# Performance work log

Measured on AMD Instinct MI355X. Metric: run time of the kernel, lower is better.

The kernel has to match this reference:

```python
import jax, jax.numpy as jnp
import numpy as np

B, R, N, D = 8, 5, 1024, 512  # batch, relations, utterances per dialogue, d_model
LN_EPS = 1e-5


def setup_inputs() -> dict:
    key = jax.random.key(0)
    k1, k2, k3 = jax.random.split(key, 3)
    h = jax.random.normal(k1, (B, N, D), dtype=jnp.float32)
    # Binary adjacency: adj[b, r, v, u] = 1 means u sends a message to v under relation r.
    adj = (jax.random.uniform(k2, (B, R, N, N)) < 0.5).astype(jnp.float32)
    # Relation 0 is the self-loop relation (identity), as in build_adjacency.
    adj = adj.at[:, 0].set(jnp.broadcast_to(jnp.eye(N, dtype=jnp.float32), (B, N, N)))
    # Per-relation Linear (bias=False) weights, torch convention: y = x @ W_r.T, W_r: (D, D)
    W = jax.random.normal(k3, (R, D, D), dtype=jnp.float32) * 0.02
    gamma = jnp.ones((D,), dtype=jnp.float32)
    beta = jnp.zeros((D,), dtype=jnp.float32)
    return {"h": h, "adj": adj, "W": W, "gamma": gamma, "beta": beta}


def reference(h, adj, W, gamma, beta):
    # Degree-normalize each relation's adjacency (row-normalized mean aggregation).
    deg = jnp.clip(jnp.sum(adj, axis=-1, keepdims=True), 1.0)  # (B,R,N,1)
    A = adj / deg
    # Mean aggregation per relation: (B,R,N,N) @ (B,N,D) -> (B,R,N,D)
    msg = jnp.einsum('brvu,bud->brvd', A, h)
    # Per-relation linear (x @ W_r.T) and sum over relations: (B,N,D)
    agg = jnp.einsum('brvd,red->bve', msg, W)
    # Dropout is identity in eval mode; ReLU, residual, LayerNorm.
    out = jax.nn.relu(agg) + h
    mu = jnp.mean(out, axis=-1, keepdims=True)
    xc = out - mu
    var = jnp.mean(xc * xc, axis=-1, keepdims=True)
    return xc / jnp.sqrt(var + LN_EPS) * gamma + beta
```

## Files before the change

### kernel.cpp

```cpp
#include <hip/hip_runtime.h>
#include <stdint.h>

#define Bd 8
#define Rr 5
#define Nn 1024
#define Dd 512
#define KK (Rr*Dd)

typedef __attribute__((ext_vector_type(8))) short bf16x8;
typedef __attribute__((ext_vector_type(4))) float f32x4;
typedef unsigned short u16;
typedef unsigned int u32;

__device__ __forceinline__ u16 f2bf(float x){
  union { float f; unsigned u; } v; v.f = x;
  unsigned r = v.u + 0x7FFFu + ((v.u >> 16) & 1u);
  return (u16)(r >> 16);
}

__global__ __launch_bounds__(256) void k_prep(
    const float* __restrict__ h, const float* __restrict__ W,
    u16* __restrict__ hTp, u16* __restrict__ Wt2p){
  __shared__ float t32[32][65];
  const int tid = threadIdx.x;
  const int g = blockIdx.x;
  if (g < 2048){
    const int ut  = g & 31;
    const int dtg = (g >> 5) & 7;
    const int b   = g >> 8;
    const float* hb = h + ((size_t)b*Nn + (size_t)ut*32)*Dd + dtg*64;
    #pragma unroll
    for (int j=0;j<8;j++){
      int e = j*256 + tid;
      int ul = e >> 6, dl = e & 63;
      t32[ul][dl] = hb[(size_t)ul*Dd + dl];
    }
    __syncthreads();
    u16* ob = hTp + (size_t)b*Dd*Nn;
    #pragma unroll
    for (int j=0;j<8;j++){
      int e = j*256 + tid;
      int dtl = e >> 9;
      int rem = e & 511;
      int dr = rem >> 5, uu = rem & 31;
      int dt = dtg*4 + dtl;
      ob[((size_t)ut*32 + dt)*512 + rem] = f2bf(t32[uu][dtl*16 + dr]);
    }
  } else {
    int q = (g - 2048)*1024 + tid*4;
    int kk = q & 31;
    int er = (q >> 5) & 15;
    int et = (q >> 9) & 31;
    int kt = q >> 14;
    int k = kt*32 + kk;
    int e = et*16 + er;
    int r, d;
    if (k < 2048){ r = 1 + (k >> 9); d = k & 511; }
    else         { r = 0;            d = k - 2048; }
    f32x4 w = *(const f32x4*)(W + (((size_t)r*Dd + e)*Dd + d));
    u16 o[4] = { f2bf(w.x), f2bf(w.y), f2bf(w.z), f2bf(w.w) };
    *(uint2*)(Wt2p + q) = *(uint2*)o;
  }
}

__global__ __launch_bounds__(512,2) void k_fused(
    const float* __restrict__ adj, const u16* __restrict__ hTp,
    const u16* __restrict__ Wt2p, const float* __restrict__ h,
    const float* __restrict__ gamma, const float* __restrict__ beta,
    float* __restrict__ out){
  __shared__ __align__(16) u16 sA[2][4][32*64];
  __shared__ __align__(16) u16 sBt[32*512];
  __shared__ float sT[16*516];
  __shared__ float sDeg[4][32];

  const int tid  = threadIdx.x;
  const int lane = tid & 63;
  const int wave = tid >> 6;
  const int b  = blockIdx.x & 7;
  const int vt = blockIdx.x >> 3;
  const int v0 = vt * 32;
  const int t0 = blockIdx.x & 15;
  const float* adjb = adj + (((size_t)b*Rr + 1)*Nn + v0)*Nn;
  const u16* hTpb = hTp + (size_t)b*Dd*Nn;

  const int srow = tid >> 4;
  const int sc   = tid & 15;
  const size_t aoff = (size_t)srow*Nn + sc*4;
  const int wslot = sc ^ ((srow & 7) << 1);

  float deg[4] = {0.f,0.f,0.f,0.f};
  f32x4 areg[4];
  f32x4 acc[4][2][4];
  #pragma unroll
  for (int ri=0;ri<4;ri++)
    #pragma unroll
    for (int m=0;m<2;m++)
      #pragma unroll
      for (int n=0;n<4;n++) acc[ri][m][n] = (f32x4){0.f,0.f,0.f,0.f};

  const int rlo = lane & 15, ch = lane >> 4;
  const int boff = rlo*32 + ch*8;

  #define TT(x) (((x) + t0) & 15)

  #define AISSUE(T) do {                                                      \
    _Pragma("unroll")                                                         \
    for (int ri=0;ri<4;ri++)                                                  \
      areg[ri] = *(const f32x4*)(adjb + (size_t)ri*Nn*Nn + (size_t)(T)*64 + aoff); \
  } while(0)

  #define PACK(BUFI) do {                                                     \
    _Pragma("unroll")                                                         \
    for (int ri=0;ri<4;ri++){                                                 \
      f32x4 p = areg[ri];                                                     \
      deg[ri] += p.x+p.y+p.z+p.w;                                             \
      uint2 pk;                           \
      pk.x = (__float_as_uint(p.x)>>16) | (__float_as_uint(p.y) & 0xFFFF0000u);\
      pk.y = (__float_as_uint(p.z)>>16) | (__float_as_uint(p.w) & 0xFFFF0000u);\
      *(uint2*)((char*)sA[BUFI][ri] + srow*128 + wslot*8) = pk;               \
    }                                                                         \
  } while(0)

  #define LOADB(T) do {                                                      \
    _Pragma("unroll")                                                         \
    for (int kk=0;kk<2;kk++){                                                 \
      const u16* bp = hTpb + ((((size_t)((T)*2+kk))*32 + (wave<<2))<<9) + boff;\
      _Pragma("unroll")                                                       \
      for (int n=0;n<4;n++)                                                   \
        bfr[kk][n] = *(const bf16x8*)(bp + ((size_t)n<<9));                   \
    }                                                                         \
  } while(0)

  #define MSTEP(BUFI) do {                                                    \
    const char* abase = (const char*)sA[BUFI];                                \
    _Pragma("unroll")                                                         \
    for (int kk=0;kk<2;kk++){                                                 \
      _Pragma("unroll")                                                       \
      for (int ri=0;ri<4;ri++){                                               \
        bf16x8 af[2];                                                         \
        _Pragma("unroll")                                                     \
        for (int m=0;m<2;m++){                                                \
          const int row = m*16 + rlo;                                         \
          af[m] = *(const bf16x8*)(abase + ri*4096 + row*128                  \
                    + (((kk*8 + ch*2) ^ ((row&7)<<1))<<3));                   \
        }                                                                     \
        _Pragma("unroll")                                                     \
        for (int m=0;m<2;m++)                                                 \
          _Pragma("unroll")                                                   \
          for (int n=0;n<4;n++)                                               \
            acc[ri][m][n] = __builtin_amdgcn_mfma_f32_16x16x32_bf16(          \
                af[m], bfr[kk][n], acc[ri][m][n], 0, 0, 0);                   \
      }                                                                       \
    }                                                                         \
  } while(0)

  #define FENCE() __builtin_amdgcn_sched_barrier(0)
  #define STEP_BARRIER() do {                                                 \
    asm volatile("s_waitcnt lgkmcnt(0)" ::: "memory");                        \
    FENCE();                                                                  \
    __builtin_amdgcn_s_barrier();                                             \
    FENCE();                                                                  \
  } while(0)

  bf16x8 bfr[2][4];

  AISSUE(TT(0));
  PACK(0);
  __syncthreads();
  LOADB(TT(0));
  FENCE();
  AISSUE(TT(1));
  FENCE();

  for (int t = 0; t < 15; ++t){
    PACK((t+1)&1);
    FENCE();
    if (t < 14) AISSUE(TT(t+2));
    FENCE();
    MSTEP(t&1);
    FENCE();
    LOADB(TT(t+1));
    STEP_BARRIER();
  }
  MSTEP(1);
  #undef TT
  #undef AISSUE
  #undef PACK
  #undef LOADB
  #undef MSTEP

  #pragma unroll
  for (int ri=0;ri<4;ri++){
    float d = deg[ri];
    d += __shfl_xor(d, 1); d += __shfl_xor(d, 2);
    d += __shfl_xor(d, 4); d += __shfl_xor(d, 8);
    if (sc == 0) sDeg[ri][srow] = d;
  }
  __syncthreads();

  f32x4 acc2[4][2];
  #pragma unroll
  for (int m=0;m<4;m++)
    #pragma unroll
    for (int n=0;n<2;n++) acc2[m][n] = (f32x4){0.f,0.f,0.f,0.f};

  #pragma unroll
  for (int p=0; p<5; ++p){
    if (p < 4){
      #pragma unroll
      for (int m=0;m<2;m++)
        #pragma unroll
        for (int reg=0;reg<4;reg++){
          const int v = m*16 + ch*4 + reg;
          const float inv = 1.0f / fmaxf(sDeg[p][v], 1.0f);
          #pragma unroll
          for (int n=0;n<4;n++){
            const int d = (wave<<6) + n*16 + rlo;
            sBt[v*512 + ((((d>>3) ^ (v&7))<<3) | (d&7))] =
                f2bf(acc[p][m][n][reg] * inv);
          }
        }
    } else {
      const int v = tid >> 4;
      const float* hp = h + ((size_t)b*Nn + v0 + v)*Dd + (tid&15)*32;
      #pragma unroll
      for (int j=0;j<4;j++){
        f32x4 a = *(const f32x4*)(hp + j*8);
        f32x4 c = *(const f32x4*)(hp + j*8 + 4);
        bf16x8 pk;
        pk[0]=(short)f2bf(a.x); pk[1]=(short)f2bf(a.y);
        pk[2]=(short)f2bf(a.z); pk[3]=(short)f2bf(a.w);
        pk[4]=(short)f2bf(c.x); pk[5]=(short)f2bf(c.y);
        pk[6]=(short)f2bf(c.z); pk[7]=(short)f2bf(c.w);
        const int d0 = (tid&15)*32 + j*8;
        *(bf16x8*)&sBt[v*512 + (((d0>>3) ^ (v&7))<<3)] = pk;
      }
    }
    __syncthreads();
    #pragma unroll
    for (int s=0; s<16; ++s){
      const int kt = p*16 + s;
      bf16x8 wfr[4], btf[2];
      #pragma unroll
      for (int m=0;m<4;m++){
        const int et = (wave<<2) + m;
        wfr[m] = *(const bf16x8*)(Wt2p + (((size_t)kt*32 + et)<<9) + boff);
      }
      #pragma unroll
      for (int n=0;n<2;n++){
        const int v = n*16 + rlo;
        btf[n] = *(const bf16x8*)&sBt[v*512 + ((((s*4 + ch) ^ (v&7)))<<3)];
      }
      #pragma unroll
      for (int m=0;m<4;m++)
        #pragma unroll
        for (int n=0;n<2;n++)
          acc2[m][n] = __builtin_amdgcn_mfma_f32_16x16x32_bf16(
              wfr[m], btf[n], acc2[m][n], 0, 0, 0);
    }
    __syncthreads();
  }

  #pragma unroll
  for (int hh=0; hh<2; ++hh){
    #pragma unroll
    for (int m=0;m<4;m++)
      #pragma unroll
      for (int reg=0;reg<4;reg++){
        const int col = (wave<<6) + m*16 + ch*4 + reg;
        const int colw = col ^ (((col>>5)&7)<<2);
        sT[rlo*516 + colw] = fmaxf(acc2[m][hh][reg], 0.f);
      }
    __syncthreads();
    {
      const int row = wave*2 + (lane>>5);
      const int elane = lane & 31;
      const int grow = v0 + hh*16 + row;
      const float* hp = h + ((size_t)b*Nn + grow)*Dd + elane*16;
      float x[16];
      float sum = 0.f, sq = 0.f;
      #pragma unroll
      for (int j=0;j<4;j++){
        const int col = elane*16 + j*4;
        const int colw = col ^ (((col>>5)&7)<<2);
        f32x4 sv = *(const f32x4*)&sT[row*516 + colw];
        f32x4 hv = *(const f32x4*)(hp + j*4);
        #pragma unroll
        for (int k=0;k<4;k++){
          float val = sv[k] + hv[k];
          x[j*4+k] = val; sum += val; sq += val*val;
        }
      }
      #pragma unroll
      for (int off=16; off; off>>=1){
        sum += __shfl_xor(sum, off);
        sq  += __shfl_xor(sq,  off);
      }
      const float mu  = sum * (1.f/(float)Dd);
      const float var = sq * (1.f/(float)Dd) - mu*mu;
      const float rstd = rsqrtf(var + 1e-5f);
      float* op = out + ((size_t)b*Nn + grow)*Dd + elane*16;
      #pragma unroll
      for (int j=0;j<4;j++){
        f32x4 g  = *(const f32x4*)(gamma + elane*16 + j*4);
        f32x4 be = *(const f32x4*)(beta  + elane*16 + j*4);
        f32x4 ov;
        #pragma unroll
        for (int k=0;k<4;k++)
          ov[k] = (x[j*4+k] - mu) * rstd * g[k] + be[k];
        *(f32x4*)(op + j*4) = ov;
      }
    }
    __syncthreads();
  }
  #undef FENCE
  #undef STEP_BARRIER
}

extern "C" void kernel_launch(void* const* d_in, const int* in_sizes, int n_in,
                              void* d_out, int out_size, void* d_ws, size_t ws_size,
                              hipStream_t stream){
  const float* h     = (const float*)d_in[0];
  const float* adj   = (const float*)d_in[1];
  const float* W     = (const float*)d_in[2];
  const float* gamma = (const float*)d_in[3];
  const float* beta  = (const float*)d_in[4];
  float* out = (float*)d_out;
  char* ws = (char*)d_ws;

  u16*  hTp  = (u16*)(ws);
  u16*  Wt2p = (u16*)(ws + 8388608);

  k_prep <<<dim3(3328), dim3(256), 0, stream>>>(h, W, hTp, Wt2p);
  k_fused<<<dim3(Bd*32), dim3(512), 0, stream>>>(adj, hTp, Wt2p, h, gamma, beta, out);
}
```

Before: 105.7 us.

## Stream adjacency tiles via global_load_lds into triple-buffered LDS ring

Replaces register-staged adjacency loads with direct global-to-LDS async loads into a 3-slot ring, issuing tiles two steps ahead and using vmcnt-based waits before each barrier. All shared buffers are merged into one large aliased LDS block (~128KB), so launch bounds drop to one block per CU. The aim is deeper prefetch of the fp32 adjacency stream and lower VGPR pressure, at the cost of occupancy and some extra LDS read traffic for packing.

```diff
diff --git a/kernel.cpp b/kernel.cpp
--- a/kernel.cpp
+++ b/kernel.cpp
@@ -16,6 +16,12 @@
   union { float f; unsigned u; } v; v.f = x;
   unsigned r = v.u + 0x7FFFu + ((v.u >> 16) & 1u);
   return (u16)(r >> 16);
+}
+
+__device__ __forceinline__ void gll16(const void* g, void* l){
+  __builtin_amdgcn_global_load_lds(
+      (const __attribute__((address_space(1))) void*)g,
+      (__attribute__((address_space(3))) void*)l, 16, 0, 0);
 }
 
 __global__ __launch_bounds__(256) void k_prep(
@@ -63,15 +69,16 @@
   }
 }
 
-__global__ __launch_bounds__(512,2) void k_fused(
+__global__ __launch_bounds__(512,1) void k_fused(
     const float* __restrict__ adj, const u16* __restrict__ hTp,
     const u16* __restrict__ Wt2p, const float* __restrict__ h,
     const float* __restrict__ gamma, const float* __restrict__ beta,
     float* __restrict__ out){
-  __shared__ __align__(16) u16 sA[2][4][32*64];
-  __shared__ __align__(16) u16 sBt[32*512];
-  __shared__ float sT[16*516];
-  __shared__ float sDeg[4][32];
+  __shared__ __align__(16) char smem[131584];
+  char* sAc = smem + 98304;
+  float (*sDeg)[32] = (float(*)[32])(smem + 131072);
+  u16* sBt = (u16*)smem;
+  float* sT = (float*)smem;
 
   const int tid  = threadIdx.x;
   const int lane = tid & 63;
@@ -85,11 +92,9 @@
 
   const int srow = tid >> 4;
   const int sc   = tid & 15;
-  const size_t aoff = (size_t)srow*Nn + sc*4;
   const int wslot = sc ^ ((srow & 7) << 1);
 
   float deg[4] = {0.f,0.f,0.f,0.f};
-  f32x4 areg[4];
   f32x4 acc[4][2][4];
   #pragma unroll
   for (int ri=0;ri<4;ri++)
@@ -103,36 +108,39 @@
 
   #define TT(x) (((x) + t0) & 15)
 
-  #define AISSUE(T) do {                                                      \
+  #define GLLA(T) do {                                                        \
+    char* _d = smem + ((T)%3)*32768 + wave*1024;                              \
     _Pragma("unroll")                                                         \
     for (int ri=0;ri<4;ri++)                                                  \
-      areg[ri] = *(const f32x4*)(adjb + (size_t)ri*Nn*Nn + (size_t)(T)*64 + aoff); \
-  } while(0)
-
-  #define PACK(BUFI) do {                                                     \
+      gll16(adjb + (size_t)ri*Nn*Nn + (size_t)TT(T)*64 + (size_t)srow*Nn + sc*4, \
+            _d + ri*8192);                                                    \
+  } while(0)
+
+  #define PACKL(T) do {                                                       \
+    const char* _s = smem + ((T)%3)*32768 + tid*16;                           \
     _Pragma("unroll")                                                         \
     for (int ri=0;ri<4;ri++){                                                 \
-      f32x4 p = areg[ri];                                                     \
+      f32x4 p = *(const f32x4*)(_s + ri*8192);                                \
       deg[ri] += p.x+p.y+p.z+p.w;                                             \
       uint2 pk;                           \
       pk.x = (__float_as_uint(p.x)>>16) | (__float_as_uint(p.y) & 0xFFFF0000u);\
       pk.y = (__float_as_uint(p.z)>>16) | (__float_as_uint(p.w) & 0xFFFF0000u);\
-      *(uint2*)((char*)sA[BUFI][ri] + srow*128 + wslot*8) = pk;               \
+      *(uint2*)(sAc + ((T)&1)*16384 + ri*4096 + srow*128 + wslot*8) = pk;     \
     }                                                                         \
   } while(0)
 
   #define LOADB(T) do {                                                      \
     _Pragma("unroll")                                                         \
     for (int kk=0;kk<2;kk++){                                                 \
-      const u16* bp = hTpb + ((((size_t)((T)*2+kk))*32 + (wave<<2))<<9) + boff;\
+      const u16* bp = hTpb + ((((size_t)(TT(T)*2+kk))*32 + (wave<<2))<<9) + boff;\
       _Pragma("unroll")                                                       \
       for (int n=0;n<4;n++)                                                   \
         bfr[kk][n] = *(const bf16x8*)(bp + ((size_t)n<<9));                   \
     }                                                                         \
   } while(0)
 
-  #define MSTEP(BUFI) do {                                                    \
-    const char* abase = (const char*)sA[BUFI];                                \
+  #define MSTEP(T) do {                                                       \
+    const char* abase = sAc + ((T)&1)*16384;                                  \
     _Pragma("unroll")                                                         \
     for (int kk=0;kk<2;kk++){                                                 \
       _Pragma("unroll")                                                       \
@@ -155,37 +163,41 @@
   } while(0)
 
   #define FENCE() __builtin_amdgcn_sched_barrier(0)
-  #define STEP_BARRIER() do {                                                 \
-    asm volatile("s_waitcnt lgkmcnt(0)" ::: "memory");                        \
-    FENCE();                                                                  \
-    __builtin_amdgcn_s_barrier();                                             \
-    FENCE();                                                                  \
+  #define WAITB12() do {                                                      \
+    asm volatile("s_waitcnt lgkmcnt(0) vmcnt(12)" ::: "memory");              \
+    FENCE(); __builtin_amdgcn_s_barrier(); FENCE();                           \
+  } while(0)
+  #define WAITB8() do {                                                       \
+    asm volatile("s_waitcnt lgkmcnt(0) vmcnt(8)" ::: "memory");               \
+    FENCE(); __builtin_amdgcn_s_barrier(); FENCE();                           \
   } while(0)
 
   bf16x8 bfr[2][4];
 
-  AISSUE(TT(0));
-  PACK(0);
-  __syncthreads();
-  LOADB(TT(0));
+  GLLA(0);
+  GLLA(1);
+  asm volatile("s_waitcnt vmcnt(4)" ::: "memory");
   FENCE();
-  AISSUE(TT(1));
-  FENCE();
-
-  for (int t = 0; t < 15; ++t){
-    PACK((t+1)&1);
+  PACKL(0);
+  LOADB(0);
+  GLLA(2);
+  WAITB12();
+
+  for (int t = 0; t < 13; ++t){
+    PACKL(t+1);
     FENCE();
-    if (t < 14) AISSUE(TT(t+2));
+    MSTEP(t);
     FENCE();
-    MSTEP(t&1);
-    FENCE();
-    LOADB(TT(t+1));
-    STEP_BARRIER();
-  }
-  MSTEP(1);
+    LOADB(t+1);
+    GLLA(t+3);
+    WAITB12();
+  }
+  PACKL(14); FENCE(); MSTEP(13); FENCE(); LOADB(14); WAITB8();
+  PACKL(15); FENCE(); MSTEP(14); FENCE(); LOADB(15); WAITB8();
+  MSTEP(15);
   #undef TT
-  #undef AISSUE
-  #undef PACK
+  #undef GLLA
+  #undef PACKL
   #undef LOADB
   #undef MSTEP
 
@@ -314,7 +326,8 @@
     __syncthreads();
   }
   #undef FENCE
-  #undef STEP_BARRIER
+  #undef WAITB12
+  #undef WAITB8
 }
 
 extern "C" void kernel_launch(void* const* d_in, const int* in_sizes, int n_in,
```

Result: no change. 107.7 us (+1.8%).

## Split fused kernel into message and aggregation kernels with bf16 msg buffer

Applied to the files above, without the earlier changes.

The fused kernel is split in two. The message-passing stage writes degree-normalized bf16 messages to a global workspace, and k_prep also writes the bf16 residual h into that buffer. A new aggregation kernel then streams the message tiles into LDS with global_load_lds double buffering and runs the W GEMM plus ReLU, residual and LayerNorm. The goal is to free LDS and registers in each kernel and pipeline the second GEMM, at the cost of an extra global round-trip for msg (about 20MB) and one more launch.

```diff
diff --git a/kernel.cpp b/kernel.cpp
--- a/kernel.cpp
+++ b/kernel.cpp
@@ -18,9 +18,15 @@
   return (u16)(r >> 16);
 }
 
+__device__ __forceinline__ void gll16(const void* g, void* l){
+  __builtin_amdgcn_global_load_lds(
+      (const __attribute__((address_space(1))) void*)g,
+      (__attribute__((address_space(3))) void*)l, 16, 0, 0);
+}
+
 __global__ __launch_bounds__(256) void k_prep(
     const float* __restrict__ h, const float* __restrict__ W,
-    u16* __restrict__ hTp, u16* __restrict__ Wt2p){
+    u16* __restrict__ hTp, u16* __restrict__ Wt2p, u16* __restrict__ msg){
   __shared__ float t32[32][65];
   const int tid = threadIdx.x;
   const int g = blockIdx.x;
@@ -46,7 +52,7 @@
       int dt = dtg*4 + dtl;
       ob[((size_t)ut*32 + dt)*512 + rem] = f2bf(t32[uu][dtl*16 + dr]);
     }
-  } else {
+  } else if (g < 3328){
     int q = (g - 2048)*1024 + tid*4;
     int kk = q & 31;
     int er = (q >> 5) & 15;
@@ -60,16 +66,25 @@
     f32x4 w = *(const f32x4*)(W + (((size_t)r*Dd + e)*Dd + d));
     u16 o[4] = { f2bf(w.x), f2bf(w.y), f2bf(w.z), f2bf(w.w) };
     *(uint2*)(Wt2p + q) = *(uint2*)o;
-  }
-}
-
-__global__ __launch_bounds__(512,2) void k_fused(
+  } else {
+    int q = g - 3328;
+    int row = q*4 + (tid >> 6);
+    int d0 = (tid & 63)*8;
+    f32x4 a = *(const f32x4*)(h + (size_t)row*Dd + d0);
+    f32x4 c = *(const f32x4*)(h + (size_t)row*Dd + d0 + 4);
+    bf16x8 pk;
+    pk[0]=(short)f2bf(a.x); pk[1]=(short)f2bf(a.y);
+    pk[2]=(short)f2bf(a.z); pk[3]=(short)f2bf(a.w);
+    pk[4]=(short)f2bf(c.x); pk[5]=(short)f2bf(c.y);
+    pk[6]=(short)f2bf(c.z); pk[7]=(short)f2bf(c.w);
+    *(bf16x8*)(msg + (size_t)row*KK + 2048 + d0) = pk;
+  }
+}
+
+__global__ __launch_bounds__(512,2) void k_msg(
     const float* __restrict__ adj, const u16* __restrict__ hTp,
-    const u16* __restrict__ Wt2p, const float* __restrict__ h,
-    const float* __restrict__ gamma, const float* __restrict__ beta,
-    float* __restrict__ out){
+    u16* __restrict__ msg){
   __shared__ __align__(16) u16 sA[2][4][32*64];
-  __shared__ __align__(16) u16 sBt[32*512];
   __shared__ float sT[16*516];
   __shared__ float sDeg[4][32];
 
@@ -188,6 +203,8 @@
   #undef PACK
   #undef LOADB
   #undef MSTEP
+  #undef FENCE
+  #undef STEP_BARRIER
 
   #pragma unroll
   for (int ri=0;ri<4;ri++){
@@ -198,69 +215,132 @@
   }
   __syncthreads();
 
+  u16* mb = msg + ((size_t)b*Nn + v0)*KK;
+  #pragma unroll
+  for (int ri=0;ri<4;ri++){
+    #pragma unroll
+    for (int hh=0;hh<2;hh++){
+      #pragma unroll
+      for (int reg=0;reg<4;reg++){
+        const int rl = ch*4 + reg;
+        const float inv = 1.0f / fmaxf(sDeg[ri][hh*16 + rl], 1.0f);
+        #pragma unroll
+        for (int n=0;n<4;n++){
+          const int col = (wave<<6) + n*16 + rlo;
+          const int colw = col ^ (((col>>5)&7)<<2);
+          sT[rl*516 + colw] = acc[ri][hh][n][reg] * inv;
+        }
+      }
+      __syncthreads();
+      #pragma unroll
+      for (int s=0;s<2;s++){
+        const int rl = wave*2 + s;
+        const int m5 = lane >> 2;
+        const int e  = m5 & 7;
+        const int j0 = (2*lane) & 7;
+        f32x4 lo = *(const f32x4*)&sT[rl*516 + (m5<<5) + (((j0  ) ^ e)<<2)];
+        f32x4 hi = *(const f32x4*)&sT[rl*516 + (m5<<5) + (((j0+1) ^ e)<<2)];
+        bf16x8 pk;
+        pk[0]=(short)f2bf(lo.x); pk[1]=(short)f2bf(lo.y);
+        pk[2]=(short)f2bf(lo.z); pk[3]=(short)f2bf(lo.w);
+        pk[4]=(short)f2bf(hi.x); pk[5]=(short)f2bf(hi.y);
+        pk[6]=(short)f2bf(hi.z); pk[7]=(short)f2bf(hi.w);
+        *(bf16x8*)(mb + (size_t)(hh*16 + rl)*KK + ri*512 + lane*8) = pk;
+      }
+      __syncthreads();
+    }
+  }
+}
+
+__global__ __launch_bounds__(512,1) void k_agg2(
+    const u16* __restrict__ msg, const u16* __restrict__ Wt2p,
+    const float* __restrict__ h, const float* __restrict__ gamma,
+    const float* __restrict__ beta, float* __restrict__ out){
+  __shared__ __align__(16) u16 sA[2][32*64];
+  __shared__ float sT[16*516];
+  const int tid = threadIdx.x;
+  const int lane = tid & 63;
+  const int wave = tid >> 6;
+  const int b  = blockIdx.x & 7;
+  const int vt = blockIdx.x >> 3;
+  const int v0 = vt * 32;
+  const u16* Ab = msg + ((size_t)b*Nn + v0)*KK;
+  const int rlo = lane & 15, ch = lane >> 4;
+  const int boff = rlo*32 + ch*8;
+
   f32x4 acc2[4][2];
   #pragma unroll
   for (int m=0;m<4;m++)
     #pragma unroll
     for (int n=0;n<2;n++) acc2[m][n] = (f32x4){0.f,0.f,0.f,0.f};
 
-  #pragma unroll
-  for (int p=0; p<5; ++p){
-    if (p < 4){
-      #pragma unroll
-      for (int m=0;m<2;m++)
-        #pragma unroll
-        for (int reg=0;reg<4;reg++){
-          const int v = m*16 + ch*4 + reg;
-          const float inv = 1.0f / fmaxf(sDeg[p][v], 1.0f);
-          #pragma unroll
-          for (int n=0;n<4;n++){
-            const int d = (wave<<6) + n*16 + rlo;
-            sBt[v*512 + ((((d>>3) ^ (v&7))<<3) | (d&7))] =
-                f2bf(acc[p][m][n][reg] * inv);
-          }
-        }
-    } else {
-      const int v = tid >> 4;
-      const float* hp = h + ((size_t)b*Nn + v0 + v)*Dd + (tid&15)*32;
-      #pragma unroll
-      for (int j=0;j<4;j++){
-        f32x4 a = *(const f32x4*)(hp + j*8);
-        f32x4 c = *(const f32x4*)(hp + j*8 + 4);
-        bf16x8 pk;
-        pk[0]=(short)f2bf(a.x); pk[1]=(short)f2bf(a.y);
-        pk[2]=(short)f2bf(a.z); pk[3]=(short)f2bf(a.w);
-        pk[4]=(short)f2bf(c.x); pk[5]=(short)f2bf(c.y);
-        pk[6]=(short)f2bf(c.z); pk[7]=(short)f2bf(c.w);
-        const int d0 = (tid&15)*32 + j*8;
-        *(bf16x8*)&sBt[v*512 + (((d0>>3) ^ (v&7))<<3)] = pk;
-      }
-    }
-    __syncthreads();
-    #pragma unroll
-    for (int s=0; s<16; ++s){
-      const int kt = p*16 + s;
-      bf16x8 wfr[4], btf[2];
-      #pragma unroll
-      for (int m=0;m<4;m++){
-        const int et = (wave<<2) + m;
-        wfr[m] = *(const bf16x8*)(Wt2p + (((size_t)kt*32 + et)<<9) + boff);
-      }
-      #pragma unroll
-      for (int n=0;n<2;n++){
-        const int v = n*16 + rlo;
-        btf[n] = *(const bf16x8*)&sBt[v*512 + ((((s*4 + ch) ^ (v&7)))<<3)];
-      }
-      #pragma unroll
-      for (int m=0;m<4;m++)
-        #pragma unroll
-        for (int n=0;n<2;n++)
-          acc2[m][n] = __builtin_amdgcn_mfma_f32_16x16x32_bf16(
-              wfr[m], btf[n], acc2[m][n], 0, 0, 0);
-    }
-    __syncthreads();
-  }
-
+  #define STAGE(buf, kt) do {                                                 \
+    if (wave < 4){                                                            \
+      int c = (wave<<6) + lane;                                               \
+      int row_ = c>>3, chg = (c&7) ^ (row_&7);                                \
+      gll16(Ab + (size_t)row_*KK + (size_t)(kt)*64 + chg*8,                   \
+            (char*)sA[buf] + (wave<<10));                                     \
+    }                                                                         \
+  } while(0)
+
+  #define LOADW(T) do {                                                      \
+    _Pragma("unroll")                                                         \
+    for (int kk=0;kk<2;kk++){                                                 \
+      const size_t kt_ = (size_t)(T)*2 + kk;                                  \
+      _Pragma("unroll")                                                       \
+      for (int m=0;m<4;m++)                                                   \
+        wfr[kk][m] = *(const bf16x8*)(Wt2p + ((kt_*32 + (wave<<2)+m)<<9) + boff);\
+    }                                                                         \
+  } while(0)
+
+  #define MSTEP(BUFI) do {                                                    \
+    const char* a = (const char*)sA[BUFI];                                    \
+    _Pragma("unroll")                                                         \
+    for (int kk=0;kk<2;kk++){                                                 \
+      bf16x8 btf[2];                                                          \
+      _Pragma("unroll")                                                       \
+      for (int n=0;n<2;n++){                                                  \
+        const int row = n*16 + rlo;                                           \
+        btf[n] = *(const bf16x8*)(a + row*128 + ((((kk<<2)+ch) ^ (row&7))<<4)); \
+      }                                                                       \
+      _Pragma("unroll")                                                       \
+      for (int m=0;m<4;m++)                                                   \
+        _Pragma("unroll")                                                     \
+        for (int n=0;n<2;n++)                                                 \
+          acc2[m][n] = __builtin_amdgcn_mfma_f32_16x16x32_bf16(               \
+              wfr[kk][m], btf[n], acc2[m][n], 0, 0, 0);                       \
+    }                                                                         \
+  } while(0)
+
+  #define FENCE() __builtin_amdgcn_sched_barrier(0)
+  #define STEP_BARRIER() do {                                                 \
+    asm volatile("s_waitcnt lgkmcnt(0) vmcnt(8)" ::: "memory");               \
+    FENCE();                                                                  \
+    __builtin_amdgcn_s_barrier();                                             \
+    FENCE();                                                                  \
+  } while(0)
+
+  bf16x8 wfr[2][4];
+
+  STAGE(0, 0);
+  __syncthreads();
+  LOADW(0);
+  FENCE();
+
+  for (int t = 0; t < 39; ++t){
+    STAGE((t+1)&1, t+1);
+    FENCE();
+    MSTEP(t&1);
+    FENCE();
+    LOADW(t+1);
+    STEP_BARRIER();
+  }
+  MSTEP(1);
+  #undef STAGE
+  #undef LOADW
+  #undef MSTEP
+
+  __syncthreads();
   #pragma unroll
   for (int hh=0; hh<2; ++hh){
     #pragma unroll
@@ -330,7 +410,9 @@
 
   u16*  hTp  = (u16*)(ws);
   u16*  Wt2p = (u16*)(ws + 8388608);
-
-  k_prep <<<dim3(3328), dim3(256), 0, stream>>>(h, W, hTp, Wt2p);
-  k_fused<<<dim3(Bd*32), dim3(512), 0, stream>>>(adj, hTp, Wt2p, h, gamma, beta, out);
-}
+  u16*  msg  = (u16*)(ws + 11010048);
+
+  k_prep<<<dim3(5376), dim3(256), 0, stream>>>(h, W, hTp, Wt2p, msg);
+  k_msg <<<dim3(Bd*32), dim3(512), 0, stream>>>(adj, hTp, msg);
+  k_agg2<<<dim3(Bd*32), dim3(512), 0, stream>>>(msg, Wt2p, h, gamma, beta, out);
+}
```

Result: faster. 99.52 us (-5.9%).
